# Kernel tuning notes

Measured on AMD Instinct MI355X. Metric: run time of the kernel, lower is better.

## Reference

```python
import jax, jax.numpy as jnp
import numpy as np

NEG_INF = -1000000000.0


def setup_inputs() -> dict:
    key = jax.random.key(0)
    k1, k2, k3, k4, k5 = jax.random.split(key, 5)
    B, L1, L2, F1, F2, A = 64, 1024, 1024, 128, 128, 128
    feature1 = jax.random.normal(k1, (B, L1, F1), dtype=jnp.float32)
    feature2 = jax.random.normal(k2, (B, L2, F2), dtype=jnp.float32)
    mask = jax.random.randint(k3, (B, L1, L2), 0, 2, dtype=jnp.int32)
    # Linear weights stored torch-style: [out_features, in_features]
    W1 = jax.random.normal(k4, (A, F1), dtype=jnp.float32) / np.sqrt(F1)
    b1 = jnp.zeros((A,), dtype=jnp.float32)
    W2 = jax.random.normal(k5, (A, F2), dtype=jnp.float32) / np.sqrt(F2)
    b2 = jnp.zeros((A,), dtype=jnp.float32)
    return {"feature1": feature1, "feature2": feature2, "mask": mask,
            "W1": W1, "b1": b1, "W2": W2, "b2": b2}


def reference(feature1, feature2, mask, W1, b1, W2, b2):
    A = W1.shape[0]
    scale = jnp.sqrt(jnp.float32(A))
    q = jnp.einsum('bld,ad->bla', feature1, W1) + b1  # [B, L1, A]
    k = jnp.einsum('bmd,ad->bma', feature2, W2) + b2  # [B, L2, A]
    a = jnp.einsum('bla,bma->blm', q, k) / scale       # [B, L1, L2]
    masked_a = jnp.where(mask == 0, NEG_INF, a)
    alpha1 = jax.nn.softmax(masked_a, axis=2)  # softmax over L2
    alpha2 = jax.nn.softmax(masked_a, axis=1)  # softmax over L1
    out1 = jnp.einsum('blm,blf->bmf', alpha2, feature1)  # [B, L2, F1]
    out2 = jnp.einsum('blm,bmf->blf', alpha1, feature2)  # [B, L1, F2]
    return (out1, out2)
```

## Files before the change

### kernel.cpp

```cpp
#include <hip/hip_runtime.h>
#include <stdint.h>

typedef _Float16 f16;
typedef f16 f16x4 __attribute__((ext_vector_type(4)));
typedef f16 f16x8 __attribute__((ext_vector_type(8)));
typedef float f32x4 __attribute__((ext_vector_type(4)));

constexpr float SCALE = 0.08838834764831845f;

__device__ __forceinline__ void glds16(const void* g, void* l) {
  __builtin_amdgcn_global_load_lds(
      (const __attribute__((address_space(1))) void*)g,
      (__attribute__((address_space(3))) void*)l, 16, 0, 0);
}
__device__ __forceinline__ void glds4(const void* g, void* l) {
  __builtin_amdgcn_global_load_lds(
      (const __attribute__((address_space(1))) void*)g,
      (__attribute__((address_space(3))) void*)l, 4, 0, 0);
}

__global__ __launch_bounds__(256) void proj_kernel(
    const float* __restrict__ f1, const float* __restrict__ f2,
    const float* __restrict__ W1, const float* __restrict__ b1,
    const float* __restrict__ W2, const float* __restrict__ b2,
    f16* __restrict__ q_h, f16* __restrict__ k_h,
    f16* __restrict__ f1t, f16* __restrict__ f2t)
{
  __shared__ f16 a_lds[128 * 128];
  __shared__ f16 w_lds[128 * 128];

  const int tid = threadIdx.x;
  const int blk = blockIdx.x;
  const bool qside = blk < 512;
  const float* feat = qside ? f1 : f2;
  const float* W    = qside ? W1 : W2;
  const float* bias = qside ? b1 : b2;
  f16* op = qside ? q_h : k_h;
  f16* ft = qside ? f1t : f2t;
  const size_t row0 = (size_t)(qside ? blk : blk - 512) * 128;

  for (int it = 0; it < 16; ++it) {
    int u = tid + it * 256;
    int r = u >> 5;
    int c4 = (u & 31) * 4;
    float4 v = *(const float4*)&feat[(row0 + r) * 128 + c4];
    f16x4 h4 = { (f16)v.x, (f16)v.y, (f16)v.z, (f16)v.w };
    int adr = r * 128 + ((((c4 >> 3) ^ (r & 7)) << 3) | (c4 & 7));
    *(f16x4*)&a_lds[adr] = h4;
    float4 wv = *(const float4*)&W[r * 128 + c4];
    f16x4 wh = { (f16)wv.x, (f16)wv.y, (f16)wv.z, (f16)wv.w };
    *(f16x4*)&w_lds[adr] = wh;
  }
  __syncthreads();

  const int w = tid >> 6, l = tid & 63, lam = l & 15, g = l >> 4;
  f32x4 acc[2][8] = {};
#pragma unroll
  for (int kc = 0; kc < 4; ++kc) {
    f16x8 a[2];
#pragma unroll
    for (int rf = 0; rf < 2; ++rf) {
      int ar = w * 32 + rf * 16 + lam;
      a[rf] = *(const f16x8*)&a_lds[ar * 128 + (((4 * kc + g) ^ (ar & 7)) << 3)];
    }
#pragma unroll
    for (int cf = 0; cf < 8; ++cf) {
      int br = cf * 16 + lam;
      f16x8 bfr = *(const f16x8*)&w_lds[br * 128 + (((4 * kc + g) ^ (br & 7)) << 3)];
      acc[0][cf] = __builtin_amdgcn_mfma_f32_16x16x32_f16(a[0], bfr, acc[0][cf], 0, 0, 0);
      acc[1][cf] = __builtin_amdgcn_mfma_f32_16x16x32_f16(a[1], bfr, acc[1][cf], 0, 0, 0);
    }
  }
#pragma unroll
  for (int cf = 0; cf < 8; ++cf) {
    int col = cf * 16 + lam;
    float bv = bias[col];
#pragma unroll
    for (int rf = 0; rf < 2; ++rf)
#pragma unroll
      for (int i = 0; i < 4; ++i) {
        size_t grow = row0 + w * 32 + rf * 16 + g * 4 + i;
        op[grow * 128 + col] = (f16)(acc[rf][cf][i] + bv);
      }
  }

  {
    const int b = (int)(row0 >> 10);
    const int l0 = (int)(row0 & 1023);
    const int f = tid >> 1;
    const int half = tid & 1;
    f16 buf[64];
#pragma unroll
    for (int j = 0; j < 64; ++j) {
      int r = half * 64 + j;
      buf[j] = a_lds[r * 128 + ((((f >> 3) ^ (r & 7)) << 3) | (f & 7))];
    }
    f16* dst = ft + ((size_t)b * 128 + f) * 1024 + l0 + half * 64;
#pragma unroll
    for (int c = 0; c < 8; ++c)
      *(f16x8*)&dst[c * 8] = *(const f16x8*)&buf[c * 8];
  }
}

template <int PASS>
__global__ __launch_bounds__(256, 2) void attn_kernel(
    const f16* __restrict__ Qh, const f16* __restrict__ Kh,
    const f16* __restrict__ Vt,
    const int* __restrict__ mask, uint32_t* __restrict__ bits_w,
    const uint32_t* __restrict__ bits_r, float* __restrict__ outp)
{
  __shared__ f16 k_lds[64 * 128];
  __shared__ f16 v_lds[128 * 64];
  __shared__ f16 p_lds[8 * 16 * 72];
  __shared__ uint32_t mb[256];

  const int tid = threadIdx.x;
  const int u = blockIdx.x;
  const int qt = (u >> 3) & 7;
  const int b = ((u >> 6) << 3) | (u & 7);
  const int w = tid >> 6, l = tid & 63, lam = l & 15, g = l >> 4;
  const size_t batch_row = (size_t)b << 10;

  f16x8 qf[2][4];
#pragma unroll
  for (int qd = 0; qd < 2; ++qd) {
    const f16* qbase = Qh + (batch_row + qt * 128 + w * 32 + qd * 16 + lam) * 128;
#pragma unroll
    for (int kc = 0; kc < 4; ++kc) qf[qd][kc] = *(const f16x8*)&qbase[kc * 32 + g * 8];
  }

  f32x4 acc[2][8] = {};
  float mrun[2][4], lrun[2][4];
#pragma unroll
  for (int qd = 0; qd < 2; ++qd)
#pragma unroll
    for (int i = 0; i < 4; ++i) { mrun[qd][i] = -__builtin_inff(); lrun[qd][i] = 0.f; }

  const f16* vtb = Vt + ((size_t)b << 17);

  int4 mreg[8];
  const int mrow = tid >> 1, mhalf = tid & 1;
  const int* msrc_base = (PASS == 0)
      ? (mask + (batch_row + qt * 128 + mrow) * 1024 + mhalf * 32) : nullptr;

  auto mload = [&](int kt_) {
    const int4* src = (const int4*)(msrc_base + kt_ * 64);
#pragma unroll
    for (int e = 0; e < 8; ++e) mreg[e] = src[e];
  };
  auto mpack = [&](int kt_) {
    uint32_t wd = 0;
#pragma unroll
    for (int e = 0; e < 8; ++e) {
      if (mreg[e].x) wd |= 1u << (e * 4 + 0);
      if (mreg[e].y) wd |= 1u << (e * 4 + 1);
      if (mreg[e].z) wd |= 1u << (e * 4 + 2);
      if (mreg[e].w) wd |= 1u << (e * 4 + 3);
    }
    mb[mrow * 2 + mhalf] = wd;
    bits_w[(batch_row + qt * 128 + mrow) * 32 + kt_ * 2 + mhalf] = wd;
  };

  if constexpr (PASS == 0) mload(0);

  for (int kt = 0; kt < 16; ++kt) {
    const int kb = kt * 64;
    __syncthreads();
    {
      const f16* kbase = Kh + (batch_row + kb) * 128;
#pragma unroll
      for (int it = 0; it < 4; ++it) {
        int slot0 = (w * 4 + it) * 64;
        int i = slot0 + l;
        int r = i >> 4, ch = i & 15;
        glds16(kbase + r * 128 + ((ch ^ (r & 7)) << 3), &k_lds[slot0 * 8]);
      }
    }
    {
#pragma unroll
      for (int it = 0; it < 4; ++it) {
        int slot0 = (w * 4 + it) * 64;
        int i = slot0 + l;
        int r = i >> 3, ch = i & 7;
        glds16(vtb + r * 1024 + kb + ((ch ^ (r & 7)) << 3), &v_lds[slot0 * 8]);
      }
    }
    if constexpr (PASS == 0) {
      mpack(kt);
    } else {
      glds4(bits_r + (batch_row + kb + w * 16 + (l >> 2)) * 32 + qt * 4 + (l & 3),
            &mb[w * 64]);
    }
    __syncthreads();

    if constexpr (PASS == 0) {
      if (kt < 15) mload(kt + 1);
    }

#pragma unroll
    for (int qd = 0; qd < 2; ++qd) {
      f32x4 sv[4] = {};
#pragma unroll
      for (int kc = 0; kc < 4; ++kc) {
#pragma unroll
        for (int cf = 0; cf < 4; ++cf) {
          int br = cf * 16 + lam;
          f16x8 bk = *(const f16x8*)&k_lds[br * 128 + (((4 * kc + g) ^ (br & 7)) << 3)];
          sv[cf] = __builtin_amdgcn_mfma_f32_16x16x32_f16(qf[qd][kc], bk, sv[cf], 0, 0, 0);
        }
      }

      uint32_t mk = 0;
      if constexpr (PASS == 0) {
#pragma unroll
        for (int i = 0; i < 4; ++i) {
          int rowi = w * 32 + qd * 16 + g * 4 + i;
          uint32_t w0 = mb[rowi * 2 + 0];
          uint32_t w1 = mb[rowi * 2 + 1];
#pragma unroll
          for (int cf = 0; cf < 4; ++cf) {
            uint32_t wd = (cf < 2) ? w0 : w1;
            mk |= ((wd >> ((cf & 1) * 16 + lam)) & 1u) << (cf * 4 + i);
          }
        }
      } else {
#pragma unroll
        for (int cf = 0; cf < 4; ++cf) {
          uint32_t wd = mb[(cf * 16 + lam) * 4 + w];
#pragma unroll
          for (int i = 0; i < 4; ++i)
            mk |= ((wd >> (qd * 16 + g * 4 + i)) & 1u) << (cf * 4 + i);
        }
      }

      float mrow4[4];
#pragma unroll
      for (int i = 0; i < 4; ++i) mrow4[i] = -1e30f;
#pragma unroll
      for (int cf = 0; cf < 4; ++cf)
#pragma unroll
        for (int i = 0; i < 4; ++i) {
          float v = sv[cf][i] * SCALE;
          sv[cf][i] = v;
          mrow4[i] = fmaxf(mrow4[i], ((mk >> (cf * 4 + i)) & 1u) ? v : -1e30f);
        }
#pragma unroll
      for (int d = 1; d <= 8; d <<= 1)
#pragma unroll
        for (int i = 0; i < 4; ++i)
          mrow4[i] = fmaxf(mrow4[i], __shfl_xor(mrow4[i], d, 64));

      float sf[4], lsum[4];
#pragma unroll
      for (int i = 0; i < 4; ++i) {
        float mn = fmaxf(mrun[qd][i], mrow4[i]);
        sf[i] = __expf(mrun[qd][i] - mn);
        mrun[qd][i] = mn;
        lsum[i] = 0.f;
      }
      f16* pslice = &p_lds[(w * 2 + qd) * 1152];
#pragma unroll
      for (int cf = 0; cf < 4; ++cf)
#pragma unroll
        for (int i = 0; i < 4; ++i) {
          float p = ((mk >> (cf * 4 + i)) & 1u) ? __expf(sv[cf][i] - mrun[qd][i]) : 0.f;
          lsum[i] += p;
          int row = g * 4 + i;
          int cchunk = 2 * cf + (lam >> 3);
          pslice[row * 72 + (((cchunk ^ (row & 7)) << 3) | (lam & 7))] = (f16)p;
        }
#pragma unroll
      for (int d = 1; d <= 8; d <<= 1)
#pragma unroll
        for (int i = 0; i < 4; ++i)
          lsum[i] += __shfl_xor(lsum[i], d, 64);
#pragma unroll
      for (int i = 0; i < 4; ++i) lrun[qd][i] = lrun[qd][i] * sf[i] + lsum[i];
#pragma unroll
      for (int nf = 0; nf < 8; ++nf)
#pragma unroll
        for (int i = 0; i < 4; ++i) acc[qd][nf][i] *= sf[i];
    }

#pragma unroll
    for (int kc2 = 0; kc2 < 2; ++kc2) {
      f16x8 ap0 = *(const f16x8*)&p_lds[(w * 2 + 0) * 1152 + lam * 72 + (((4 * kc2 + g) ^ (lam & 7)) << 3)];
      f16x8 ap1 = *(const f16x8*)&p_lds[(w * 2 + 1) * 1152 + lam * 72 + (((4 * kc2 + g) ^ (lam & 7)) << 3)];
#pragma unroll
      for (int nf = 0; nf < 8; ++nf) {
        int vr = nf * 16 + lam;
        f16x8 bv = *(const f16x8*)&v_lds[vr * 64 + (((kc2 * 4 + g) ^ (vr & 7)) << 3)];
        acc[0][nf] = __builtin_amdgcn_mfma_f32_16x16x32_f16(ap0, bv, acc[0][nf], 0, 0, 0);
        acc[1][nf] = __builtin_amdgcn_mfma_f32_16x16x32_f16(ap1, bv, acc[1][nf], 0, 0, 0);
      }
    }
  }

#pragma unroll
  for (int qd = 0; qd < 2; ++qd) {
    float inv[4];
#pragma unroll
    for (int i = 0; i < 4; ++i) inv[i] = (lrun[qd][i] > 0.f) ? 1.f / lrun[qd][i] : 0.f;
    const size_t orow0 = batch_row + (size_t)qt * 128 + w * 32 + qd * 16;
#pragma unroll
    for (int nf = 0; nf < 8; ++nf)
#pragma unroll
      for (int i = 0; i < 4; ++i)
        outp[(orow0 + g * 4 + i) * 128 + nf * 16 + lam] = acc[qd][nf][i] * inv[i];
  }
}

extern "C" void kernel_launch(void* const* d_in, const int* in_sizes, int n_in,
                              void* d_out, int out_size, void* d_ws, size_t ws_size,
                              hipStream_t stream) {
  const float* f1 = (const float*)d_in[0];
  const float* f2 = (const float*)d_in[1];
  const int* mask = (const int*)d_in[2];
  const float* W1 = (const float*)d_in[3];
  const float* b1 = (const float*)d_in[4];
  const float* W2 = (const float*)d_in[5];
  const float* b2 = (const float*)d_in[6];
  float* out = (float*)d_out;

  if (ws_size < (size_t)3 * 8388608 * sizeof(f16) + 8388608) return;

  f16* q_h = (f16*)d_ws;
  f16* k_h = q_h + 8388608;
  f16* f1t = k_h + 8388608;
  uint32_t* bits = (uint32_t*)(f1t + 8388608);
  f16* f2t = (f16*)d_out;

  proj_kernel<<<1024, 256, 0, stream>>>(f1, f2, W1, b1, W2, b2, q_h, k_h, f1t, f2t);
  attn_kernel<0><<<512, 256, 0, stream>>>(q_h, k_h, f2t, mask, bits, nullptr,
                                          out + 8388608);
  attn_kernel<1><<<512, 256, 0, stream>>>(k_h, q_h, f1t, nullptr, nullptr, bits,
                                          out);
}
```

Measured before the change: 255.0 us.

## Double-buffer K/V/mask LDS tiles, shrink P buffer, add setprio and nontemporal IO

The attention kernel now double-buffers the K, V and mask-bit tiles in LDS. The next tile's async global-to-LDS loads are issued right after a single barrier, so they overlap the current tile's MFMA work, where before each iteration waited behind two barriers. The P·V product is moved inside the qd loop so only one P slice per wave is kept, which halves p_lds and partly offsets the larger K/V buffers. It also adds s_setprio around the MFMA blocks and uses nontemporal loads for features and mask and nontemporal stores for the output, trading higher LDS use for less exposed load latency.

```diff
diff --git a/kernel.cpp b/kernel.cpp
--- a/kernel.cpp
+++ b/kernel.cpp
@@ -5,6 +5,7 @@
 typedef f16 f16x4 __attribute__((ext_vector_type(4)));
 typedef f16 f16x8 __attribute__((ext_vector_type(8)));
 typedef float f32x4 __attribute__((ext_vector_type(4)));
+typedef int i32x4 __attribute__((ext_vector_type(4)));
 
 constexpr float SCALE = 0.08838834764831845f;
 
@@ -43,8 +44,9 @@
     int u = tid + it * 256;
     int r = u >> 5;
     int c4 = (u & 31) * 4;
-    float4 v = *(const float4*)&feat[(row0 + r) * 128 + c4];
-    f16x4 h4 = { (f16)v.x, (f16)v.y, (f16)v.z, (f16)v.w };
+    f32x4 v = __builtin_nontemporal_load(
+        (const f32x4*)&feat[(row0 + r) * 128 + c4]);
+    f16x4 h4 = { (f16)v[0], (f16)v[1], (f16)v[2], (f16)v[3] };
     int adr = r * 128 + ((((c4 >> 3) ^ (r & 7)) << 3) | (c4 & 7));
     *(f16x4*)&a_lds[adr] = h4;
     float4 wv = *(const float4*)&W[r * 128 + c4];
@@ -105,14 +107,13 @@
 template <int PASS>
 __global__ __launch_bounds__(256, 2) void attn_kernel(
     const f16* __restrict__ Qh, const f16* __restrict__ Kh,
-    const f16* __restrict__ Vt,
-    const int* __restrict__ mask, uint32_t* __restrict__ bits_w,
-    const uint32_t* __restrict__ bits_r, float* __restrict__ outp)
+    const f16* __restrict__ Vt, const int* __restrict__ mask,
+    uint32_t* __restrict__ bits, float* __restrict__ outp)
 {
-  __shared__ f16 k_lds[64 * 128];
-  __shared__ f16 v_lds[128 * 64];
-  __shared__ f16 p_lds[8 * 16 * 72];
-  __shared__ uint32_t mb[256];
+  __shared__ f16 k_lds[2][64 * 128];
+  __shared__ f16 v_lds[2][128 * 64];
+  __shared__ f16 p_lds[4 * 16 * 72];
+  __shared__ uint32_t mb[2][256];
 
   const int tid = threadIdx.x;
   const int u = blockIdx.x;
@@ -120,6 +121,7 @@
   const int b = ((u >> 6) << 3) | (u & 7);
   const int w = tid >> 6, l = tid & 63, lam = l & 15, g = l >> 4;
   const size_t batch_row = (size_t)b << 10;
+  const f16* vtb = Vt + ((size_t)b << 17);
 
   f16x8 qf[2][4];
 #pragma unroll
@@ -129,6 +131,53 @@
     for (int kc = 0; kc < 4; ++kc) qf[qd][kc] = *(const f16x8*)&qbase[kc * 32 + g * 8];
   }
 
+  auto stageKV = [&](int kt_, int bu) {
+    const int kb_ = kt_ * 64;
+    const f16* kbase = Kh + (batch_row + kb_) * 128;
+#pragma unroll
+    for (int it = 0; it < 4; ++it) {
+      int slot0 = (w * 4 + it) * 64;
+      int i = slot0 + l;
+      int r = i >> 4, ch = i & 15;
+      glds16(kbase + r * 128 + ((ch ^ (r & 7)) << 3), &k_lds[bu][slot0 * 8]);
+    }
+#pragma unroll
+    for (int it = 0; it < 4; ++it) {
+      int slot0 = (w * 4 + it) * 64;
+      int i = slot0 + l;
+      int r = i >> 3, ch = i & 7;
+      glds16(vtb + r * 1024 + kb_ + ((ch ^ (r & 7)) << 3), &v_lds[bu][slot0 * 8]);
+    }
+  };
+  auto stageBits = [&](int kt_, int bu) {
+    int idx = w * 64 + l;
+    glds4(bits + (batch_row + kt_ * 64 + (idx >> 2)) * 32 + qt * 4 + (l & 3),
+          &mb[bu][w * 64]);
+  };
+
+  i32x4 mreg[8];
+  const int mrow = tid >> 1, mhalf = tid & 1;
+  const i32x4* msrc = (PASS == 0)
+      ? (const i32x4*)(mask + (batch_row + qt * 128 + mrow) * 1024 + mhalf * 32)
+      : nullptr;
+  auto mload = [&](int kt_) {
+#pragma unroll
+    for (int e = 0; e < 8; ++e)
+      mreg[e] = __builtin_nontemporal_load(msrc + kt_ * 16 + e);
+  };
+  auto mpack = [&](int kt_, int bu) {
+    uint32_t wd = 0;
+#pragma unroll
+    for (int e = 0; e < 8; ++e) {
+      if (mreg[e][0]) wd |= 1u << (e * 4 + 0);
+      if (mreg[e][1]) wd |= 1u << (e * 4 + 1);
+      if (mreg[e][2]) wd |= 1u << (e * 4 + 2);
+      if (mreg[e][3]) wd |= 1u << (e * 4 + 3);
+    }
+    mb[bu][mrow * 2 + mhalf] = wd;
+    bits[(batch_row + qt * 128 + mrow) * 32 + kt_ * 2 + mhalf] = wd;
+  };
+
   f32x4 acc[2][8] = {};
   float mrun[2][4], lrun[2][4];
 #pragma unroll
@@ -136,87 +185,45 @@
 #pragma unroll
     for (int i = 0; i < 4; ++i) { mrun[qd][i] = -__builtin_inff(); lrun[qd][i] = 0.f; }
 
-  const f16* vtb = Vt + ((size_t)b << 17);
-
-  int4 mreg[8];
-  const int mrow = tid >> 1, mhalf = tid & 1;
-  const int* msrc_base = (PASS == 0)
-      ? (mask + (batch_row + qt * 128 + mrow) * 1024 + mhalf * 32) : nullptr;
-
-  auto mload = [&](int kt_) {
-    const int4* src = (const int4*)(msrc_base + kt_ * 64);
-#pragma unroll
-    for (int e = 0; e < 8; ++e) mreg[e] = src[e];
-  };
-  auto mpack = [&](int kt_) {
-    uint32_t wd = 0;
-#pragma unroll
-    for (int e = 0; e < 8; ++e) {
-      if (mreg[e].x) wd |= 1u << (e * 4 + 0);
-      if (mreg[e].y) wd |= 1u << (e * 4 + 1);
-      if (mreg[e].z) wd |= 1u << (e * 4 + 2);
-      if (mreg[e].w) wd |= 1u << (e * 4 + 3);
-    }
-    mb[mrow * 2 + mhalf] = wd;
-    bits_w[(batch_row + qt * 128 + mrow) * 32 + kt_ * 2 + mhalf] = wd;
-  };
-
   if constexpr (PASS == 0) mload(0);
-
+  stageKV(0, 0);
+  if constexpr (PASS == 1) stageBits(0, 0);
+
+  int c = 0;
   for (int kt = 0; kt < 16; ++kt) {
-    const int kb = kt * 64;
     __syncthreads();
-    {
-      const f16* kbase = Kh + (batch_row + kb) * 128;
-#pragma unroll
-      for (int it = 0; it < 4; ++it) {
-        int slot0 = (w * 4 + it) * 64;
-        int i = slot0 + l;
-        int r = i >> 4, ch = i & 15;
-        glds16(kbase + r * 128 + ((ch ^ (r & 7)) << 3), &k_lds[slot0 * 8]);
-      }
-    }
-    {
-#pragma unroll
-      for (int it = 0; it < 4; ++it) {
-        int slot0 = (w * 4 + it) * 64;
-        int i = slot0 + l;
-        int r = i >> 3, ch = i & 7;
-        glds16(vtb + r * 1024 + kb + ((ch ^ (r & 7)) << 3), &v_lds[slot0 * 8]);
-      }
-    }
-    if constexpr (PASS == 0) {
-      mpack(kt);
-    } else {
-      glds4(bits_r + (batch_row + kb + w * 16 + (l >> 2)) * 32 + qt * 4 + (l & 3),
-            &mb[w * 64]);
-    }
-    __syncthreads();
-
-    if constexpr (PASS == 0) {
-      if (kt < 15) mload(kt + 1);
+
+    if constexpr (PASS == 0) mpack(kt, c);
+
+    if (kt < 15) {
+      if constexpr (PASS == 0) mload(kt + 1);
+      stageKV(kt + 1, c ^ 1);
+      if constexpr (PASS == 1) stageBits(kt + 1, c ^ 1);
+      asm volatile("" ::: "memory");
     }
 
 #pragma unroll
     for (int qd = 0; qd < 2; ++qd) {
       f32x4 sv[4] = {};
+      __builtin_amdgcn_s_setprio(1);
 #pragma unroll
       for (int kc = 0; kc < 4; ++kc) {
 #pragma unroll
         for (int cf = 0; cf < 4; ++cf) {
           int br = cf * 16 + lam;
-          f16x8 bk = *(const f16x8*)&k_lds[br * 128 + (((4 * kc + g) ^ (br & 7)) << 3)];
+          f16x8 bk = *(const f16x8*)&k_lds[c][br * 128 + (((4 * kc + g) ^ (br & 7)) << 3)];
           sv[cf] = __builtin_amdgcn_mfma_f32_16x16x32_f16(qf[qd][kc], bk, sv[cf], 0, 0, 0);
         }
       }
+      __builtin_amdgcn_s_setprio(0);
 
       uint32_t mk = 0;
       if constexpr (PASS == 0) {
 #pragma unroll
         for (int i = 0; i < 4; ++i) {
           int rowi = w * 32 + qd * 16 + g * 4 + i;
-          uint32_t w0 = mb[rowi * 2 + 0];
-          uint32_t w1 = mb[rowi * 2 + 1];
+          uint32_t w0 = mb[c][rowi * 2 + 0];
+          uint32_t w1 = mb[c][rowi * 2 + 1];
 #pragma unroll
           for (int cf = 0; cf < 4; ++cf) {
             uint32_t wd = (cf < 2) ? w0 : w1;
@@ -226,7 +233,7 @@
       } else {
 #pragma unroll
         for (int cf = 0; cf < 4; ++cf) {
-          uint32_t wd = mb[(cf * 16 + lam) * 4 + w];
+          uint32_t wd = mb[c][(cf * 16 + lam) * 4 + w];
 #pragma unroll
           for (int i = 0; i < 4; ++i)
             mk |= ((wd >> (qd * 16 + g * 4 + i)) & 1u) << (cf * 4 + i);
@@ -258,7 +265,7 @@
         mrun[qd][i] = mn;
         lsum[i] = 0.f;
       }
-      f16* pslice = &p_lds[(w * 2 + qd) * 1152];
+      f16* pslice = &p_lds[w * 1152];
 #pragma unroll
       for (int cf = 0; cf < 4; ++cf)
 #pragma unroll
@@ -280,20 +287,21 @@
       for (int nf = 0; nf < 8; ++nf)
 #pragma unroll
         for (int i = 0; i < 4; ++i) acc[qd][nf][i] *= sf[i];
-    }
-
-#pragma unroll
-    for (int kc2 = 0; kc2 < 2; ++kc2) {
-      f16x8 ap0 = *(const f16x8*)&p_lds[(w * 2 + 0) * 1152 + lam * 72 + (((4 * kc2 + g) ^ (lam & 7)) << 3)];
-      f16x8 ap1 = *(const f16x8*)&p_lds[(w * 2 + 1) * 1152 + lam * 72 + (((4 * kc2 + g) ^ (lam & 7)) << 3)];
-#pragma unroll
-      for (int nf = 0; nf < 8; ++nf) {
-        int vr = nf * 16 + lam;
-        f16x8 bv = *(const f16x8*)&v_lds[vr * 64 + (((kc2 * 4 + g) ^ (vr & 7)) << 3)];
-        acc[0][nf] = __builtin_amdgcn_mfma_f32_16x16x32_f16(ap0, bv, acc[0][nf], 0, 0, 0);
-        acc[1][nf] = __builtin_amdgcn_mfma_f32_16x16x32_f16(ap1, bv, acc[1][nf], 0, 0, 0);
-      }
-    }
+
+      __builtin_amdgcn_s_setprio(1);
+#pragma unroll
+      for (int kc2 = 0; kc2 < 2; ++kc2) {
+        f16x8 ap = *(const f16x8*)&pslice[lam * 72 + (((4 * kc2 + g) ^ (lam & 7)) << 3)];
+#pragma unroll
+        for (int nf = 0; nf < 8; ++nf) {
+          int vr = nf * 16 + lam;
+          f16x8 bv = *(const f16x8*)&v_lds[c][vr * 64 + (((kc2 * 4 + g) ^ (vr & 7)) << 3)];
+          acc[qd][nf] = __builtin_amdgcn_mfma_f32_16x16x32_f16(ap, bv, acc[qd][nf], 0, 0, 0);
+        }
+      }
+      __builtin_amdgcn_s_setprio(0);
+    }
+    c ^= 1;
   }
 
 #pragma unroll
@@ -306,7 +314,8 @@
     for (int nf = 0; nf < 8; ++nf)
 #pragma unroll
       for (int i = 0; i < 4; ++i)
-        outp[(orow0 + g * 4 + i) * 128 + nf * 16 + lam] = acc[qd][nf][i] * inv[i];
+        __builtin_nontemporal_store(acc[qd][nf][i] * inv[i],
+            &outp[(orow0 + g * 4 + i) * 128 + nf * 16 + lam]);
   }
 }
 
@@ -331,8 +340,8 @@
   f16* f2t = (f16*)d_out;
 
   proj_kernel<<<1024, 256, 0, stream>>>(f1, f2, W1, b1, W2, b2, q_h, k_h, f1t, f2t);
-  attn_kernel<0><<<512, 256, 0, stream>>>(q_h, k_h, f2t, mask, bits, nullptr,
+  attn_kernel<0><<<512, 256, 0, stream>>>(q_h, k_h, f2t, mask, bits,
                                           out + 8388608);
-  attn_kernel<1><<<512, 256, 0, stream>>>(k_h, q_h, f1t, nullptr, nullptr, bits,
+  attn_kernel<1><<<512, 256, 0, stream>>>(k_h, q_h, f1t, nullptr, bits,
                                           out);
 }
```

Result: slower. 311.3 us (+22.1%).
